# Kernel optimization log

Measured on AMD Instinct MI355X. Metric: run time of the kernel, lower is better.

## Reference

```python
import jax, jax.numpy as jnp
import numpy as np

N_EMBD = 1024
N_HEAD = 16
HEAD_SIZE = N_EMBD // N_HEAD
B, T = 2, 2048
LN_EPS = 1e-5


def _layernorm(x, g, b):
    mu = jnp.mean(x, axis=-1, keepdims=True)
    var = jnp.var(x, axis=-1, keepdims=True)
    return (x - mu) * jax.lax.rsqrt(var + LN_EPS) * g + b


def setup_inputs() -> dict:
    key = jax.random.key(0)
    ks = jax.random.split(key, 12)
    s_in = 1.0 / np.sqrt(N_EMBD)
    s_ff = 1.0 / np.sqrt(4 * N_EMBD)
    return {
        "x": jax.random.normal(ks[0], (B, T, N_EMBD), jnp.float32),
        # per-head q/k/v linears stacked head-major: [n_embd, n_embd]
        "Wq": jax.random.uniform(ks[1], (N_EMBD, N_EMBD), jnp.float32, -s_in, s_in),
        "Wk": jax.random.uniform(ks[2], (N_EMBD, N_EMBD), jnp.float32, -s_in, s_in),
        "Wv": jax.random.uniform(ks[3], (N_EMBD, N_EMBD), jnp.float32, -s_in, s_in),
        "Wo": jax.random.uniform(ks[4], (N_EMBD, N_EMBD), jnp.float32, -s_in, s_in),
        "bo": jax.random.uniform(ks[5], (N_EMBD,), jnp.float32, -s_in, s_in),
        "W1": jax.random.uniform(ks[6], (N_EMBD, 4 * N_EMBD), jnp.float32, -s_in, s_in),
        "b1": jax.random.uniform(ks[7], (4 * N_EMBD,), jnp.float32, -s_in, s_in),
        "W2": jax.random.uniform(ks[8], (4 * N_EMBD, N_EMBD), jnp.float32, -s_ff, s_ff),
        "b2": jax.random.uniform(ks[9], (N_EMBD,), jnp.float32, -s_ff, s_ff),
        "g1": jnp.ones((N_EMBD,), jnp.float32),
        "be1": jnp.zeros((N_EMBD,), jnp.float32),
        "g2": jnp.ones((N_EMBD,), jnp.float32),
        "be2": jnp.zeros((N_EMBD,), jnp.float32),
    }


def reference(x, Wq, Wk, Wv, Wo, bo, W1, b1, W2, b2, g1, be1, g2, be2):
    Bx, Tx, C = x.shape
    # --- self-attention on ln1(x) ---
    h = _layernorm(x, g1, be1)
    q = (h @ Wq).reshape(Bx, Tx, N_HEAD, HEAD_SIZE)
    k = (h @ Wk).reshape(Bx, Tx, N_HEAD, HEAD_SIZE)
    v = (h @ Wv).reshape(Bx, Tx, N_HEAD, HEAD_SIZE)
    # NOTE: faithful to source -- scale uses full C (n_embd), not head_size
    scale = C ** (-0.5)
    wei = jnp.einsum("bqhd,bkhd->bhqk", q, k) * scale  # [B,H,T,T]
    causal = jnp.tril(jnp.ones((Tx, Tx), bool))
    wei = jnp.where(causal, wei, -jnp.inf)
    wei = jax.nn.softmax(wei, axis=-1)
    attn = jnp.einsum("bhqk,bkhd->bqhd", wei, v).reshape(Bx, Tx, C)
    x = x + (attn @ Wo + bo)
    # --- feed-forward on ln2(x) ---
    h2 = _layernorm(x, g2, be2)
    x = x + (jax.nn.relu(h2 @ W1 + b1) @ W2 + b2)
    return x
```

## Files before the change

### kernel.cpp

```cpp
#include <hip/hip_runtime.h>
#include <hip/hip_bf16.h>
#include <math.h>

#define BB 2
#define TT 2048
#define CC 1024
#define NH 16
#define HD 64
#define BT (BB*TT)
#define LN_EPS 1e-5f
#define ATT_SCALE 0.03125f

typedef __bf16 bf16x8 __attribute__((ext_vector_type(8)));
typedef __bf16 bf16x4 __attribute__((ext_vector_type(4)));
typedef short shortx4 __attribute__((ext_vector_type(4)));
typedef float floatx4 __attribute__((ext_vector_type(4)));

__device__ __forceinline__ void gl_lds16(const __bf16* g, __bf16* l) {
    __builtin_amdgcn_global_load_lds((const __attribute__((address_space(1))) void*)g,
                                     (__attribute__((address_space(3))) void*)l,
                                     16, 0, 0);
}

#define MFMA32(a, b, c) __builtin_amdgcn_mfma_f32_16x16x32_bf16(a, b, c, 0, 0, 0)

#if __has_builtin(__builtin_amdgcn_mfma_f32_16x16x16_bf16)
__device__ __forceinline__ floatx4 mfma16(bf16x4 a, bf16x4 b, floatx4 c) {
    return __builtin_amdgcn_mfma_f32_16x16x16_bf16(a, b, c, 0, 0, 0);
}
#else
__device__ __forceinline__ floatx4 mfma16(bf16x4 a, bf16x4 b, floatx4 c) {
    return __builtin_amdgcn_mfma_f32_16x16x16bf16_1k(
        __builtin_bit_cast(shortx4, a), __builtin_bit_cast(shortx4, b), c, 0, 0, 0);
}
#endif

__device__ __forceinline__ void swizzle_xcd(int& xb, int& yb, int& zb) {
    int nx = gridDim.x, ny = gridDim.y;
    int total = nx * ny * (int)gridDim.z;
    int lin = blockIdx.x + nx * (blockIdx.y + ny * blockIdx.z);
    int c = lin & 7, s = lin >> 3;
    int idx = c * (total >> 3) + s;
    xb = idx % nx;
    yb = (idx / nx) % ny;
    zb = idx / (nx * ny);
}

__global__ __launch_bounds__(256) void ln_kernel(const float* __restrict__ x,
                                                 const float* __restrict__ g,
                                                 const float* __restrict__ b,
                                                 __bf16* __restrict__ out) {
    int row = blockIdx.x;
    const float4* xr = (const float4*)(x + (size_t)row * CC);
    float4 v = xr[threadIdx.x];
    float s  = v.x + v.y + v.z + v.w;
    float ss = v.x*v.x + v.y*v.y + v.z*v.z + v.w*v.w;
    #pragma unroll
    for (int off = 32; off; off >>= 1) {
        s  += __shfl_down(s, off);
        ss += __shfl_down(ss, off);
    }
    __shared__ float rs_[4], rss_[4];
    __shared__ float mu_s, inv_s;
    int lane = threadIdx.x & 63, wid = threadIdx.x >> 6;
    if (lane == 0) { rs_[wid] = s; rss_[wid] = ss; }
    __syncthreads();
    if (threadIdx.x == 0) {
        float S  = rs_[0] + rs_[1] + rs_[2] + rs_[3];
        float SS = rss_[0] + rss_[1] + rss_[2] + rss_[3];
        float mu  = S * (1.0f / CC);
        float var = SS * (1.0f / CC) - mu * mu;
        mu_s  = mu;
        inv_s = rsqrtf(var + LN_EPS);
    }
    __syncthreads();
    float mu = mu_s, inv = inv_s;
    float4 gv = ((const float4*)g)[threadIdx.x];
    float4 bv = ((const float4*)b)[threadIdx.x];
    bf16x4 o;
    o[0] = (__bf16)((v.x - mu) * inv * gv.x + bv.x);
    o[1] = (__bf16)((v.y - mu) * inv * gv.y + bv.y);
    o[2] = (__bf16)((v.z - mu) * inv * gv.z + bv.z);
    o[3] = (__bf16)((v.w - mu) * inv * gv.w + bv.w);
    *(bf16x4*)(out + (size_t)row * CC + threadIdx.x * 4) = o;
}

__global__ __launch_bounds__(256) void reduce_wo_ln(const __bf16* __restrict__ P,
                                                    const float* __restrict__ bo,
                                                    const float* __restrict__ x,
                                                    const float* __restrict__ g2,
                                                    const float* __restrict__ be2,
                                                    float* __restrict__ x2,
                                                    __bf16* __restrict__ hb) {
    int row = blockIdx.x;
    int c = threadIdx.x * 4;
    bf16x4 a0 = *(const bf16x4*)(P + (size_t)row * CC + c);
    bf16x4 a1 = *(const bf16x4*)(P + (size_t)BT * CC + (size_t)row * CC + c);
    float4 xb = *(const float4*)(x + (size_t)row * CC + c);
    float4 bb = *(const float4*)(bo + c);
    float4 v;
    v.x = xb.x + bb.x + (float)a0[0] + (float)a1[0];
    v.y = xb.y + bb.y + (float)a0[1] + (float)a1[1];
    v.z = xb.z + bb.z + (float)a0[2] + (float)a1[2];
    v.w = xb.w + bb.w + (float)a0[3] + (float)a1[3];
    *(float4*)(x2 + (size_t)row * CC + c) = v;

    float s  = v.x + v.y + v.z + v.w;
    float ss = v.x*v.x + v.y*v.y + v.z*v.z + v.w*v.w;
    #pragma unroll
    for (int off = 32; off; off >>= 1) {
        s  += __shfl_down(s, off);
        ss += __shfl_down(ss, off);
    }
    __shared__ float rs_[4], rss_[4];
    __shared__ float mu_s, inv_s;
    int lane = threadIdx.x & 63, wid = threadIdx.x >> 6;
    if (lane == 0) { rs_[wid] = s; rss_[wid] = ss; }
    __syncthreads();
    if (threadIdx.x == 0) {
        float S  = rs_[0] + rs_[1] + rs_[2] + rs_[3];
        float SS = rss_[0] + rss_[1] + rss_[2] + rss_[3];
        float mu  = S * (1.0f / CC);
        float var = SS * (1.0f / CC) - mu * mu;
        mu_s  = mu;
        inv_s = rsqrtf(var + LN_EPS);
    }
    __syncthreads();
    float mu = mu_s, inv = inv_s;
    float4 gv = ((const float4*)g2)[threadIdx.x];
    float4 bv = ((const float4*)be2)[threadIdx.x];
    bf16x4 o;
    o[0] = (__bf16)((v.x - mu) * inv * gv.x + bv.x);
    o[1] = (__bf16)((v.y - mu) * inv * gv.y + bv.y);
    o[2] = (__bf16)((v.z - mu) * inv * gv.z + bv.z);
    o[3] = (__bf16)((v.w - mu) * inv * gv.w + bv.w);
    *(bf16x4*)(hb + (size_t)row * CC + c) = o;
}

__global__ __launch_bounds__(256) void reduce_ffn(const __bf16* __restrict__ P,
                                                  const float* __restrict__ b2,
                                                  const float* __restrict__ x2,
                                                  float* __restrict__ out) {
    int row = blockIdx.x;
    int c = threadIdx.x * 4;
    const size_t S = (size_t)BT * CC;
    float4 v = *(const float4*)(x2 + (size_t)row * CC + c);
    float4 bb = *(const float4*)(b2 + c);
    v.x += bb.x; v.y += bb.y; v.z += bb.z; v.w += bb.w;
    #pragma unroll
    for (int z = 0; z < 4; ++z) {
        bf16x4 a = *(const bf16x4*)(P + z * S + (size_t)row * CC + c);
        v.x += (float)a[0]; v.y += (float)a[1]; v.z += (float)a[2]; v.w += (float)a[3];
    }
    *(float4*)(out + (size_t)row * CC + c) = v;
}

__global__ __launch_bounds__(256) void transpose_all(
        const float* __restrict__ Wq, const float* __restrict__ Wk,
        const float* __restrict__ Wv, const float* __restrict__ Wo,
        const float* __restrict__ W1, const float* __restrict__ W2,
        __bf16* __restrict__ WqkvT, __bf16* __restrict__ WoT,
        __bf16* __restrict__ W1T, __bf16* __restrict__ W2T) {
    int idx = blockIdx.x;
    const float* src; __bf16* dst; int K, N, tn, tk;
    if (idx < 3072) {
        int wsel = idx >> 10, local = idx & 1023;
        src = (wsel == 0) ? Wq : (wsel == 1 ? Wk : Wv);
        dst = WqkvT + (size_t)wsel * 1024 * 1024;
        K = 1024; N = 1024; tn = local & 31; tk = local >> 5;
    } else if (idx < 4096) {
        int local = idx - 3072;
        src = Wo; dst = WoT; K = 1024; N = 1024; tn = local & 31; tk = local >> 5;
    } else if (idx < 8192) {
        int local = idx - 4096;
        src = W1; dst = W1T; K = 1024; N = 4096; tn = local & 127; tk = local >> 7;
    } else {
        int local = idx - 8192;
        src = W2; dst = W2T; K = 4096; N = 1024; tn = local & 31; tk = local >> 5;
    }
    __shared__ float t[32][33];
    int n0 = tn * 32, k0 = tk * 32;
    int tx = threadIdx.x & 31, ty = threadIdx.x >> 5;
    #pragma unroll
    for (int r = ty; r < 32; r += 8)
        t[r][tx] = src[(size_t)(k0 + r) * N + n0 + tx];
    __syncthreads();
    #pragma unroll
    for (int r = ty; r < 32; r += 8)
        dst[(size_t)(n0 + r) * K + k0 + tx] = (__bf16)t[tx][r];
}

template<int NT, int SK, typename OT, bool BIAS, bool RELU, bool RES, bool VSPLIT>
__global__ __launch_bounds__(256) void gemm_bf16(const __bf16* __restrict__ A,
                                                 const __bf16* __restrict__ Bt,
                                                 const float* __restrict__ bias,
                                                 const float* __restrict__ res,
                                                 OT* __restrict__ C,
                                                 __bf16* __restrict__ vt,
                                                 int M, int N, int K) {
    constexpr int JN = NT / 32;
    __shared__ __bf16 As[128 * 32];
    __shared__ __bf16 Bs[NT * 32];
    int bx, by, bz;
    swizzle_xcd(bx, by, bz);
    const int tid = threadIdx.x;
    const int l = tid & 63, w = tid >> 6;
    const int m = l & 15, g = l >> 4;
    const int wm = w >> 1, wn = w & 1;
    const int m0 = by * 128, n0 = bx * NT;
    const int Keff = K / SK;
    const int kbase = (SK > 1) ? bz * Keff : 0;

    const int srow = w * 16 + (l >> 2);
    const int skof = (l & 3) * 8;
    const __bf16* ga = A  + (size_t)(m0 + srow) * K + kbase + skof;
    const __bf16* gb = Bt + (size_t)(n0 + srow) * K + kbase + skof;
    __bf16* la0 = As + w * 512;
    __bf16* lb0 = Bs + w * 512;

    floatx4 acc[4][JN];
    #pragma unroll
    for (int i = 0; i < 4; ++i)
        #pragma unroll
        for (int j = 0; j < JN; ++j) {
            floatx4 z = {0.f, 0.f, 0.f, 0.f};
            acc[i][j] = z;
        }

    for (int kt = 0; kt < Keff; kt += 32) {
        __syncthreads();
        gl_lds16(ga,                  la0);
        gl_lds16(ga + (size_t)64 * K, la0 + 2048);
        gl_lds16(gb,                  lb0);
        if (NT == 128)
            gl_lds16(gb + (size_t)64 * K, lb0 + 2048);
        ga += 32; gb += 32;
        __syncthreads();

        bf16x8 af[4], bfr[JN];
        #pragma unroll
        for (int i = 0; i < 4; ++i)
            af[i] = *(const bf16x8*)&As[(wm * 64 + i * 16 + m) * 32 + g * 8];
        #pragma unroll
        for (int j = 0; j < JN; ++j)
            bfr[j] = *(const bf16x8*)&Bs[(wn * (NT / 2) + j * 16 + m) * 32 + g * 8];
        #pragma unroll
        for (int i = 0; i < 4; ++i)
            #pragma unroll
            for (int j = 0; j < JN; ++j)
                acc[i][j] = MFMA32(af[i], bfr[j], acc[i][j]);
    }

    if (SK > 1) {
        __bf16* P = (__bf16*)C + (size_t)bz * M * N;
        #pragma unroll
        for (int i = 0; i < 4; ++i) {
            int row = m0 + wm * 64 + i * 16 + g * 4;
            #pragma unroll
            for (int j = 0; j < JN; ++j) {
                int col = n0 + wn * (NT / 2) + j * 16 + m;
                #pragma unroll
                for (int r = 0; r < 4; ++r)
                    P[(size_t)(row + r) * N + col] = (__bf16)acc[i][j][r];
            }
        }
    } else if (VSPLIT && n0 >= 2048) {
        #pragma unroll
        for (int i = 0; i < 4; ++i) {
            int row = m0 + wm * 64 + i * 16 + g * 4;
            int bb = row >> 11, t0 = row & 2047;
            #pragma unroll
            for (int j = 0; j < JN; ++j) {
                int cv = n0 + wn * (NT / 2) + j * 16 + m - 2048;
                bf16x4 o;
                #pragma unroll
                for (int r = 0; r < 4; ++r) o[r] = (__bf16)acc[i][j][r];
                *(bf16x4*)(vt + ((size_t)(bb * NH + (cv >> 6)) * HD + (cv & 63)) * 2048 + t0) = o;
            }
        }
    } else {
        #pragma unroll
        for (int i = 0; i < 4; ++i) {
            int row = m0 + wm * 64 + i * 16 + g * 4;
            #pragma unroll
            for (int j = 0; j < JN; ++j) {
                int col = n0 + wn * (NT / 2) + j * 16 + m;
                float bv = BIAS ? bias[col] : 0.0f;
                #pragma unroll
                for (int r = 0; r < 4; ++r) {
                    float vo = acc[i][j][r] + bv;
                    if (RELU) vo = fmaxf(vo, 0.0f);
                    if (RES)  vo += res[(size_t)(row + r) * N + col];
                    C[(size_t)(row + r) * N + col] = (OT)vo;
                }
            }
        }
    }
}

__global__ __launch_bounds__(256, 2) void attn_mfma3(const __bf16* __restrict__ qkv,
                                                     const __bf16* __restrict__ vt,
                                                     __bf16* __restrict__ att) {
    const int lin = blockIdx.x;
    const int half = lin >> 8, pid = lin & 255;
    const int q0 = pid & 7, h = (pid >> 3) & 15, b = pid >> 7;
    const int qt = half ? 15 - q0 : q0;

    const int tid = threadIdx.x;
    const int l = tid & 63, w = tid >> 6;
    const int m = l & 15, g = l >> 4;

    __shared__ __bf16 Ks[2][128][32];
    __shared__ __bf16 Vt3[8][64][16];

    const __bf16* qp = qkv + (size_t)b * TT * 3072 + h * HD;
    const __bf16* kp = qp + 1024;
    const __bf16* vh = vt + (size_t)(b * NH + h) * HD * 2048;

    bf16x8 qb[2][2];
    #pragma unroll
    for (int nt = 0; nt < 2; ++nt) {
        int qrow = qt * 128 + w * 32 + nt * 16 + m;
        qb[nt][0] = *(const bf16x8*)(qp + (size_t)qrow * 3072 + g * 8);
        qb[nt][1] = *(const bf16x8*)(qp + (size_t)qrow * 3072 + 32 + g * 8);
    }

    floatx4 O[2][4];
    float l_s[2] = {0.0f, 0.0f};
    #pragma unroll
    for (int nt = 0; nt < 2; ++nt)
        #pragma unroll
        for (int jd = 0; jd < 4; ++jd) {
            floatx4 z = {0.f, 0.f, 0.f, 0.f};
            O[nt][jd] = z;
        }

    for (int kt = 0; kt <= qt; ++kt) {
        __syncthreads();
        #pragma unroll
        for (int c = 0; c < 4; ++c) {
            int idx = w * 4 + c;
            int dh = idx >> 3, k16 = idx & 7;
            gl_lds16(kp + (size_t)(kt * 128 + k16 * 16 + (l >> 2)) * 3072
                        + dh * 32 + (((l & 3) ^ ((l >> 3) & 3)) * 8),
                     (__bf16*)Ks + dh * 4096 + k16 * 512);
        }
        #pragma unroll
        for (int c = 0; c < 4; ++c) {
            int idx = w * 4 + c;
            int jt = idx >> 1, dhf = idx & 1;
            gl_lds16(vh + (size_t)(dhf * 32 + (l >> 1)) * 2048 + kt * 128
                        + jt * 16 + (((l & 1) ^ ((l >> 3) & 1)) * 8),
                     (__bf16*)Vt3 + jt * 1024 + dhf * 512);
        }
        __syncthreads();

        floatx4 S[2][8];
        #pragma unroll
        for (int jt = 0; jt < 8; ++jt) {
            int co = (g ^ ((m >> 1) & 3)) * 8;
            bf16x8 kf0 = *(const bf16x8*)&Ks[0][jt * 16 + m][co];
            bf16x8 kf1 = *(const bf16x8*)&Ks[1][jt * 16 + m][co];
            #pragma unroll
            for (int nt = 0; nt < 2; ++nt) {
                floatx4 z = {0.f, 0.f, 0.f, 0.f};
                z = MFMA32(kf0, qb[nt][0], z);
                S[nt][jt] = MFMA32(kf1, qb[nt][1], z);
            }
        }

        bf16x4 pv[2][8];
        const bool last = (kt == qt);
        #pragma unroll
        for (int nt = 0; nt < 2; ++nt) {
            if (last) {
                int qr = w * 32 + nt * 16 + m;
                #pragma unroll
                for (int jt = 0; jt < 8; ++jt)
                    #pragma unroll
                    for (int r = 0; r < 4; ++r)
                        if (jt * 16 + g * 4 + r > qr) S[nt][jt][r] = -1e30f;
            }
            float ls = 0.0f;
            #pragma unroll
            for (int jt = 0; jt < 8; ++jt) {
                bf16x4 t;
                #pragma unroll
                for (int r = 0; r < 4; ++r) {
                    float p = __expf(S[nt][jt][r] * ATT_SCALE);
                    ls += p;
                    t[r] = (__bf16)p;
                }
                pv[nt][jt] = t;
            }
            l_s[nt] += ls;
        }

        #pragma unroll
        for (int jt = 0; jt < 8; ++jt)
            #pragma unroll
            for (int jd = 0; jd < 4; ++jd) {
                bf16x4 vf = *(const bf16x4*)&Vt3[jt][jd * 16 + m]
                                [((g >> 1) ^ ((m >> 2) & 1)) * 8 + (g & 1) * 4];
                #pragma unroll
                for (int nt = 0; nt < 2; ++nt)
                    O[nt][jd] = mfma16(vf, pv[nt][jt], O[nt][jd]);
            }
    }

    #pragma unroll
    for (int nt = 0; nt < 2; ++nt) {
        float lsum = l_s[nt];
        lsum += __shfl_xor(lsum, 16, 64);
        lsum += __shfl_xor(lsum, 32, 64);
        float inv = 1.0f / lsum;
        int qrow = qt * 128 + w * 32 + nt * 16 + m;
        #pragma unroll
        for (int jd = 0; jd < 4; ++jd) {
            bf16x4 o;
            #pragma unroll
            for (int r = 0; r < 4; ++r) o[r] = (__bf16)(O[nt][jd][r] * inv);
            *(bf16x4*)(att + ((size_t)b * TT + qrow) * CC + h * HD + jd * 16 + g * 4) = o;
        }
    }
}

extern "C" void kernel_launch(void* const* d_in, const int* in_sizes, int n_in,
                              void* d_out, int out_size, void* d_ws, size_t ws_size,
                              hipStream_t stream) {
    const float* x   = (const float*)d_in[0];
    const float* Wq  = (const float*)d_in[1];
    const float* Wk  = (const float*)d_in[2];
    const float* Wv  = (const float*)d_in[3];
    const float* Wo  = (const float*)d_in[4];
    const float* bo  = (const float*)d_in[5];
    const float* W1  = (const float*)d_in[6];
    const float* b1  = (const float*)d_in[7];
    const float* W2  = (const float*)d_in[8];
    const float* b2  = (const float*)d_in[9];
    const float* g1  = (const float*)d_in[10];
    const float* be1 = (const float*)d_in[11];
    const float* g2  = (const float*)d_in[12];
    const float* be2 = (const float*)d_in[13];
    float* out = (float*)d_out;

    char* p = (char*)d_ws;
    char*   pool  = p;          p += (size_t)32 * 1024 * 1024;
    __bf16* qkvb  = (__bf16*)pool;
    __bf16* vtb   = (__bf16*)(pool + (size_t)BT * 3072 * 2);
    __bf16* wop   = (__bf16*)pool;
    __bf16* ffp   = (__bf16*)pool;
    __bf16* attb  = (__bf16*)p; p += (size_t)BT * CC * 2;
    __bf16* hb    = (__bf16*)p; p += (size_t)BT * CC * 2;
    float*  x2    = (float*)p;  p += (size_t)BT * CC * 4;
    __bf16* ffb   = (__bf16*)p; p += (size_t)BT * 4096 * 2;
    __bf16* WqkvT = (__bf16*)p; p += (size_t)3072 * 1024 * 2;
    __bf16* WoT   = (__bf16*)p; p += (size_t)1024 * 1024 * 2;
    __bf16* W1T   = (__bf16*)p; p += (size_t)4096 * 1024 * 2;
    __bf16* W2T   = (__bf16*)p; p += (size_t)1024 * 4096 * 2;

    transpose_all<<<12288, 256, 0, stream>>>(Wq, Wk, Wv, Wo, W1, W2,
                                             WqkvT, WoT, W1T, W2T);
    ln_kernel<<<BT, 256, 0, stream>>>(x, g1, be1, hb);
    gemm_bf16<128, 1, __bf16, false, false, false, true><<<dim3(24, 32), 256, 0, stream>>>(
        hb, WqkvT, nullptr, nullptr, qkvb, vtb, BT, 3072, 1024);
    attn_mfma3<<<512, 256, 0, stream>>>(qkvb, vtb, attb);
    gemm_bf16<64, 2, __bf16, false, false, false, false><<<dim3(16, 32, 2), 256, 0, stream>>>(
        attb, WoT, nullptr, nullptr, wop, nullptr, BT, 1024, 1024);
    reduce_wo_ln<<<BT, 256, 0, stream>>>(wop, bo, x, g2, be2, x2, hb);
    gemm_bf16<128, 1, __bf16, true, true, false, false><<<dim3(32, 32), 256, 0, stream>>>(
        hb, W1T, b1, nullptr, ffb, nullptr, BT, 4096, 1024);
    gemm_bf16<128, 4, __bf16, false, false, false, false><<<dim3(8, 32, 4), 256, 0, stream>>>(
        ffb, W2T, nullptr, nullptr, ffp, nullptr, BT, 1024, 4096);
    reduce_ffn<<<BT, 256, 0, stream>>>(ffp, b2, x2, out);
}
```

Measured before the change: 366.4 us.

## Deepen GEMM K-tile to 64 with XOR-swizzled LDS and fuse LN into transpose

The GEMM main loop now stages 64-wide K slices per iteration instead of 32, using an XOR swizzle on the LDS column chunks so fragment reads avoid bank conflicts. This halves the number of barrier pairs per K and doubles LDS footprint per block. Separately, the first layernorm is merged into the weight-transpose kernel as extra blocks, removing one launch. Larger LDS use may reduce occupancy.

```diff
diff --git a/kernel.cpp b/kernel.cpp
--- a/kernel.cpp
+++ b/kernel.cpp
@@ -46,43 +46,77 @@
     zb = idx / (nx * ny);
 }
 
-__global__ __launch_bounds__(256) void ln_kernel(const float* __restrict__ x,
-                                                 const float* __restrict__ g,
-                                                 const float* __restrict__ b,
-                                                 __bf16* __restrict__ out) {
-    int row = blockIdx.x;
-    const float4* xr = (const float4*)(x + (size_t)row * CC);
-    float4 v = xr[threadIdx.x];
-    float s  = v.x + v.y + v.z + v.w;
-    float ss = v.x*v.x + v.y*v.y + v.z*v.z + v.w*v.w;
-    #pragma unroll
-    for (int off = 32; off; off >>= 1) {
-        s  += __shfl_down(s, off);
-        ss += __shfl_down(ss, off);
-    }
+__global__ __launch_bounds__(256) void transpose_ln(
+        const float* __restrict__ Wq, const float* __restrict__ Wk,
+        const float* __restrict__ Wv, const float* __restrict__ Wo,
+        const float* __restrict__ W1, const float* __restrict__ W2,
+        __bf16* __restrict__ WqkvT, __bf16* __restrict__ WoT,
+        __bf16* __restrict__ W1T, __bf16* __restrict__ W2T,
+        const float* __restrict__ x, const float* __restrict__ g1,
+        const float* __restrict__ be1, __bf16* __restrict__ hb) {
+    __shared__ float t[32][33];
     __shared__ float rs_[4], rss_[4];
     __shared__ float mu_s, inv_s;
-    int lane = threadIdx.x & 63, wid = threadIdx.x >> 6;
-    if (lane == 0) { rs_[wid] = s; rss_[wid] = ss; }
+    int idx = blockIdx.x;
+    if (idx >= 12288) {
+        int row = idx - 12288;
+        const float4* xr = (const float4*)(x + (size_t)row * CC);
+        float4 v = xr[threadIdx.x];
+        float s  = v.x + v.y + v.z + v.w;
+        float ss = v.x*v.x + v.y*v.y + v.z*v.z + v.w*v.w;
+        #pragma unroll
+        for (int off = 32; off; off >>= 1) {
+            s  += __shfl_down(s, off);
+            ss += __shfl_down(ss, off);
+        }
+        int lane = threadIdx.x & 63, wid = threadIdx.x >> 6;
+        if (lane == 0) { rs_[wid] = s; rss_[wid] = ss; }
+        __syncthreads();
+        if (threadIdx.x == 0) {
+            float S  = rs_[0] + rs_[1] + rs_[2] + rs_[3];
+            float SS = rss_[0] + rss_[1] + rss_[2] + rss_[3];
+            float mu  = S * (1.0f / CC);
+            float var = SS * (1.0f / CC) - mu * mu;
+            mu_s  = mu;
+            inv_s = rsqrtf(var + LN_EPS);
+        }
+        __syncthreads();
+        float mu = mu_s, inv = inv_s;
+        float4 gv = ((const float4*)g1)[threadIdx.x];
+        float4 bv = ((const float4*)be1)[threadIdx.x];
+        bf16x4 o;
+        o[0] = (__bf16)((v.x - mu) * inv * gv.x + bv.x);
+        o[1] = (__bf16)((v.y - mu) * inv * gv.y + bv.y);
+        o[2] = (__bf16)((v.z - mu) * inv * gv.z + bv.z);
+        o[3] = (__bf16)((v.w - mu) * inv * gv.w + bv.w);
+        *(bf16x4*)(hb + (size_t)row * CC + threadIdx.x * 4) = o;
+        return;
+    }
+    const float* src; __bf16* dst; int K, N, tn, tk;
+    if (idx < 3072) {
+        int wsel = idx >> 10, local = idx & 1023;
+        src = (wsel == 0) ? Wq : (wsel == 1 ? Wk : Wv);
+        dst = WqkvT + (size_t)wsel * 1024 * 1024;
+        K = 1024; N = 1024; tn = local & 31; tk = local >> 5;
+    } else if (idx < 4096) {
+        int local = idx - 3072;
+        src = Wo; dst = WoT; K = 1024; N = 1024; tn = local & 31; tk = local >> 5;
+    } else if (idx < 8192) {
+        int local = idx - 4096;
+        src = W1; dst = W1T; K = 1024; N = 4096; tn = local & 127; tk = local >> 7;
+    } else {
+        int local = idx - 8192;
+        src = W2; dst = W2T; K = 4096; N = 1024; tn = local & 31; tk = local >> 5;
+    }
+    int n0 = tn * 32, k0 = tk * 32;
+    int tx = threadIdx.x & 31, ty = threadIdx.x >> 5;
+    #pragma unroll
+    for (int r = ty; r < 32; r += 8)
+        t[r][tx] = src[(size_t)(k0 + r) * N + n0 + tx];
     __syncthreads();
-    if (threadIdx.x == 0) {
-        float S  = rs_[0] + rs_[1] + rs_[2] + rs_[3];
-        float SS = rss_[0] + rss_[1] + rss_[2] + rss_[3];
-        float mu  = S * (1.0f / CC);
-        float var = SS * (1.0f / CC) - mu * mu;
-        mu_s  = mu;
-        inv_s = rsqrtf(var + LN_EPS);
-    }
-    __syncthreads();
-    float mu = mu_s, inv = inv_s;
-    float4 gv = ((const float4*)g)[threadIdx.x];
-    float4 bv = ((const float4*)b)[threadIdx.x];
-    bf16x4 o;
-    o[0] = (__bf16)((v.x - mu) * inv * gv.x + bv.x);
-    o[1] = (__bf16)((v.y - mu) * inv * gv.y + bv.y);
-    o[2] = (__bf16)((v.z - mu) * inv * gv.z + bv.z);
-    o[3] = (__bf16)((v.w - mu) * inv * gv.w + bv.w);
-    *(bf16x4*)(out + (size_t)row * CC + threadIdx.x * 4) = o;
+    #pragma unroll
+    for (int r = ty; r < 32; r += 8)
+        dst[(size_t)(n0 + r) * K + k0 + tx] = (__bf16)t[tx][r];
 }
 
 __global__ __launch_bounds__(256) void reduce_wo_ln(const __bf16* __restrict__ P,
@@ -155,41 +189,6 @@
     *(float4*)(out + (size_t)row * CC + c) = v;
 }
 
-__global__ __launch_bounds__(256) void transpose_all(
-        const float* __restrict__ Wq, const float* __restrict__ Wk,
-        const float* __restrict__ Wv, const float* __restrict__ Wo,
-        const float* __restrict__ W1, const float* __restrict__ W2,
-        __bf16* __restrict__ WqkvT, __bf16* __restrict__ WoT,
-        __bf16* __restrict__ W1T, __bf16* __restrict__ W2T) {
-    int idx = blockIdx.x;
-    const float* src; __bf16* dst; int K, N, tn, tk;
-    if (idx < 3072) {
-        int wsel = idx >> 10, local = idx & 1023;
-        src = (wsel == 0) ? Wq : (wsel == 1 ? Wk : Wv);
-        dst = WqkvT + (size_t)wsel * 1024 * 1024;
-        K = 1024; N = 1024; tn = local & 31; tk = local >> 5;
-    } else if (idx < 4096) {
-        int local = idx - 3072;
-        src = Wo; dst = WoT; K = 1024; N = 1024; tn = local & 31; tk = local >> 5;
-    } else if (idx < 8192) {
-        int local = idx - 4096;
-        src = W1; dst = W1T; K = 1024; N = 4096; tn = local & 127; tk = local >> 7;
-    } else {
-        int local = idx - 8192;
-        src = W2; dst = W2T; K = 4096; N = 1024; tn = local & 31; tk = local >> 5;
-    }
-    __shared__ float t[32][33];
-    int n0 = tn * 32, k0 = tk * 32;
-    int tx = threadIdx.x & 31, ty = threadIdx.x >> 5;
-    #pragma unroll
-    for (int r = ty; r < 32; r += 8)
-        t[r][tx] = src[(size_t)(k0 + r) * N + n0 + tx];
-    __syncthreads();
-    #pragma unroll
-    for (int r = ty; r < 32; r += 8)
-        dst[(size_t)(n0 + r) * K + k0 + tx] = (__bf16)t[tx][r];
-}
-
 template<int NT, int SK, typename OT, bool BIAS, bool RELU, bool RES, bool VSPLIT>
 __global__ __launch_bounds__(256) void gemm_bf16(const __bf16* __restrict__ A,
                                                  const __bf16* __restrict__ Bt,
@@ -199,8 +198,8 @@
                                                  __bf16* __restrict__ vt,
                                                  int M, int N, int K) {
     constexpr int JN = NT / 32;
-    __shared__ __bf16 As[128 * 32];
-    __shared__ __bf16 Bs[NT * 32];
+    __shared__ __bf16 As[128 * 64];
+    __shared__ __bf16 Bs[NT * 64];
     int bx, by, bz;
     swizzle_xcd(bx, by, bz);
     const int tid = threadIdx.x;
@@ -211,12 +210,8 @@
     const int Keff = K / SK;
     const int kbase = (SK > 1) ? bz * Keff : 0;
 
-    const int srow = w * 16 + (l >> 2);
-    const int skof = (l & 3) * 8;
-    const __bf16* ga = A  + (size_t)(m0 + srow) * K + kbase + skof;
-    const __bf16* gb = Bt + (size_t)(n0 + srow) * K + kbase + skof;
-    __bf16* la0 = As + w * 512;
-    __bf16* lb0 = Bs + w * 512;
+    const int srow = l >> 3;
+    const int sko  = ((l & 7) ^ ((l >> 3) & 7)) * 8;
 
     floatx4 acc[4][JN];
     #pragma unroll
@@ -227,28 +222,38 @@
             acc[i][j] = z;
         }
 
-    for (int kt = 0; kt < Keff; kt += 32) {
-        __syncthreads();
-        gl_lds16(ga,                  la0);
-        gl_lds16(ga + (size_t)64 * K, la0 + 2048);
-        gl_lds16(gb,                  lb0);
-        if (NT == 128)
-            gl_lds16(gb + (size_t)64 * K, lb0 + 2048);
-        ga += 32; gb += 32;
-        __syncthreads();
-
-        bf16x8 af[4], bfr[JN];
-        #pragma unroll
-        for (int i = 0; i < 4; ++i)
-            af[i] = *(const bf16x8*)&As[(wm * 64 + i * 16 + m) * 32 + g * 8];
-        #pragma unroll
-        for (int j = 0; j < JN; ++j)
-            bfr[j] = *(const bf16x8*)&Bs[(wn * (NT / 2) + j * 16 + m) * 32 + g * 8];
-        #pragma unroll
-        for (int i = 0; i < 4; ++i)
+    for (int kt = 0; kt < Keff; kt += 64) {
+        __syncthreads();
+        #pragma unroll
+        for (int c = 0; c < 4; ++c) {
+            int idx = w * 4 + c;
+            gl_lds16(A + (size_t)(m0 + idx * 8 + srow) * K + kbase + kt + sko,
+                     As + idx * 512);
+        }
+        #pragma unroll
+        for (int c = 0; c < JN; ++c) {
+            int idx = w * JN + c;
+            gl_lds16(Bt + (size_t)(n0 + idx * 8 + srow) * K + kbase + kt + sko,
+                     Bs + idx * 512);
+        }
+        __syncthreads();
+
+        #pragma unroll
+        for (int hf = 0; hf < 2; ++hf) {
+            const int co = (((hf * 4 + g) ^ (m & 7)) * 8);
+            bf16x8 af[4], bfr[JN];
+            #pragma unroll
+            for (int i = 0; i < 4; ++i)
+                af[i] = *(const bf16x8*)&As[(wm * 64 + i * 16 + m) * 64 + co];
             #pragma unroll
             for (int j = 0; j < JN; ++j)
-                acc[i][j] = MFMA32(af[i], bfr[j], acc[i][j]);
+                bfr[j] = *(const bf16x8*)&Bs[(wn * (NT / 2) + j * 16 + m) * 64 + co];
+            #pragma unroll
+            for (int i = 0; i < 4; ++i)
+                #pragma unroll
+                for (int j = 0; j < JN; ++j)
+                    acc[i][j] = MFMA32(af[i], bfr[j], acc[i][j]);
+        }
     }
 
     if (SK > 1) {
@@ -459,9 +464,9 @@
     __bf16* W1T   = (__bf16*)p; p += (size_t)4096 * 1024 * 2;
     __bf16* W2T   = (__bf16*)p; p += (size_t)1024 * 4096 * 2;
 
-    transpose_all<<<12288, 256, 0, stream>>>(Wq, Wk, Wv, Wo, W1, W2,
-                                             WqkvT, WoT, W1T, W2T);
-    ln_kernel<<<BT, 256, 0, stream>>>(x, g1, be1, hb);
+    transpose_ln<<<16384, 256, 0, stream>>>(Wq, Wk, Wv, Wo, W1, W2,
+                                            WqkvT, WoT, W1T, W2T,
+                                            x, g1, be1, hb);
     gemm_bf16<128, 1, __bf16, false, false, false, true><<<dim3(24, 32), 256, 0, stream>>>(
         hb, WqkvT, nullptr, nullptr, qkvb, vtb, BT, 3072, 1024);
     attn_mfma3<<<512, 256, 0, stream>>>(qkvb, vtb, attb);
```

Result: faster. 335.0 us (-8.6%).
